# Kernel tuning notes

Hardware: AMD Instinct MI355X
Metric: run time of the kernel (lower is better)

Reference implementation:

```python
import jax, jax.numpy as jnp
import numpy as np

B, T, C = 2, 2048, 2048
NH, NKV = 16, 16
HD = C // NH            # 128
GATE_CH = 32
ROPE_BASE = 10000.0


def setup_inputs() -> dict:
    key = jax.random.key(0)
    ks = jax.random.split(key, 8)
    x = jax.random.normal(ks[0], (B, T, C), jnp.float32)
    ve = jax.random.normal(ks[1], (B, T, C), jnp.float32)
    # RoPE tables: half-dim rotation, shape broadcastable to [B, T, H, HD//2]
    d2 = HD // 2
    inv_freq = 1.0 / (ROPE_BASE ** (jnp.arange(d2, dtype=jnp.float32) / d2))
    angles = jnp.arange(T, dtype=jnp.float32)[:, None] * inv_freq[None, :]  # [T, d2]
    cos = jnp.cos(angles)[None, :, None, :]  # [1, T, 1, d2]
    sin = jnp.sin(angles)[None, :, None, :]
    s = 0.02
    Wq = jax.random.normal(ks[2], (C, NH * HD), jnp.float32) * s
    Wk = jax.random.normal(ks[3], (C, NKV * HD), jnp.float32) * s
    Wv = jax.random.normal(ks[4], (C, NKV * HD), jnp.float32) * s
    Wgate = jax.random.normal(ks[5], (GATE_CH, NKV), jnp.float32) * s
    Wproj = jax.random.normal(ks[6], (NH * HD, C), jnp.float32) * s
    return {"x": x, "ve": ve, "cos": cos, "sin": sin,
            "Wq": Wq, "Wk": Wk, "Wv": Wv, "Wgate": Wgate, "Wproj": Wproj}


def _apply_rotary(x, cos, sin):
    d = x.shape[3] // 2
    x1, x2 = x[..., :d], x[..., d:]
    return jnp.concatenate([x1 * cos + x2 * sin, x1 * -sin + x2 * cos], axis=3)


def _rms_norm(x):
    return x * jax.lax.rsqrt(jnp.mean(x * x, axis=-1, keepdims=True) + 1e-6)


def reference(x, ve, cos, sin, Wq, Wk, Wv, Wgate, Wproj):
    b, t, c = x.shape
    q = (x @ Wq).reshape(b, t, NH, HD)
    k = (x @ Wk).reshape(b, t, NKV, HD)
    v = (x @ Wv).reshape(b, t, NKV, HD)
    # value-embedding gate
    ve_r = ve.reshape(b, t, NKV, HD)
    gate = 2.0 * jax.nn.sigmoid(x[..., :GATE_CH] @ Wgate)  # [B, T, NKV]
    v = v + gate[..., None] * ve_r
    # RoPE then QK-RMSNorm
    q = _rms_norm(_apply_rotary(q, cos, sin))
    k = _rms_norm(_apply_rotary(k, cos, sin))
    # causal attention, scale = 1/sqrt(head_dim)
    scale = 1.0 / np.sqrt(HD).astype(np.float32)
    scores = jnp.einsum('bqhd,bkhd->bhqk', q, k) * scale
    causal = jnp.tril(jnp.ones((t, t), dtype=bool))
    scores = jnp.where(causal, scores, jnp.finfo(scores.dtype).min)
    probs = jax.nn.softmax(scores, axis=-1)
    y = jnp.einsum('bhqk,bkhd->bqhd', probs, v)
    y = y.reshape(b, t, NH * HD)
    return y @ Wproj
```

## Files before the change

### kernel.cpp

```cpp
#include <hip/hip_runtime.h>
#include <stdint.h>

typedef short bf16x8 __attribute__((ext_vector_type(8)));
typedef float f32x4 __attribute__((ext_vector_type(4)));

#define ASYNC16(g, l) __builtin_amdgcn_global_load_lds( \
    (const __attribute__((address_space(1))) unsigned int*)(g), \
    (__attribute__((address_space(3))) unsigned int*)(l), 16, 0, 0)

__device__ __forceinline__ float bf2f(short u) {
  union { unsigned int i; float f; } v;
  v.i = ((unsigned int)(unsigned short)u) << 16;
  return v.f;
}
__device__ __forceinline__ short f2bf(float f) {
  union { float f; unsigned int i; } v;
  v.f = f;
  return (short)(unsigned short)((v.i + 0x8000u) >> 16);
}
__device__ __forceinline__ float ldf(const void* p, long i, int isbf) {
  return isbf ? bf2f(((const short*)p)[i]) : ((const float*)p)[i];
}

__global__ void detect_dtype(const short* __restrict__ x, int* __restrict__ flag) {
  if (threadIdx.x == 0 && blockIdx.x == 0) {
    int cnt = 0;
    for (int i = 0; i < 128; ++i) {
      int e = (((unsigned short)x[i]) >> 7) & 0xFF;
      if (e >= 110 && e <= 136) ++cnt;
    }
    *flag = (cnt >= 120) ? 1 : 0;
  }
}

__global__ __launch_bounds__(256) void convert_x(
    const void* __restrict__ xin, short* __restrict__ xb, const int* __restrict__ flag) {
  long i = (long)blockIdx.x * 2048 + (long)threadIdx.x * 8;
  if (*flag) {
    *(bf16x8*)(xb + i) = *(const bf16x8*)((const short*)xin + i);
  } else {
    const float* xf = (const float*)xin;
    short tmp[8];
    #pragma unroll
    for (int j = 0; j < 8; ++j) tmp[j] = f2bf(xf[i + j]);
    *(bf16x8*)(xb + i) = *(bf16x8*)tmp;
  }
}

__global__ __launch_bounds__(256) void transpose_w(
    const void* __restrict__ S0, short* __restrict__ D0,
    const void* __restrict__ S1, short* __restrict__ D1,
    const void* __restrict__ S2, short* __restrict__ D2,
    const int* __restrict__ flag)
{
  int z = blockIdx.z;
  const void* S = (z == 0) ? S0 : (z == 1) ? S1 : S2;
  short* D = (z == 0) ? D0 : (z == 1) ? D1 : D2;
  int isbf = *flag;
  __shared__ short tile[32][33];
  int c0 = blockIdx.x * 32, r0 = blockIdx.y * 32;
  int tx = threadIdx.x, ty = threadIdx.y;
  #pragma unroll
  for (int i = 0; i < 4; ++i)
    tile[ty + 8*i][tx] = f2bf(ldf(S, (long)(r0 + ty + 8*i) * 2048 + c0 + tx, isbf));
  __syncthreads();
  #pragma unroll
  for (int i = 0; i < 4; ++i)
    D[(long)(c0 + ty + 8*i) * 2048 + r0 + tx] = tile[tx][ty + 8*i];
}

__global__ __launch_bounds__(256) void transpose_v(
    const short* __restrict__ Vr, short* __restrict__ Vt)
{
  __shared__ short tile[32][33];
  int bh = blockIdx.z;
  int b = bh >> 4, h = bh & 15;
  int t0 = blockIdx.x * 32, d0 = blockIdx.y * 32;
  int tx = threadIdx.x, ty = threadIdx.y;
  #pragma unroll
  for (int i = 0; i < 4; ++i)
    tile[ty + 8*i][tx] = Vr[(long)(b*2048 + t0 + ty + 8*i) * 2048 + h*128 + d0 + tx];
  __syncthreads();
  #pragma unroll
  for (int i = 0; i < 4; ++i)
    Vt[((long)bh * 128 + d0 + ty + 8*i) * 2048 + t0 + tx] = tile[tx][ty + 8*i];
}

template<typename OutT>
__global__ __launch_bounds__(256) void gemm_bt(
    const short* __restrict__ A,
    const short* __restrict__ B0, const short* __restrict__ B1, const short* __restrict__ B2,
    OutT* __restrict__ C0, OutT* __restrict__ C1, OutT* __restrict__ C2,
    int M, int N, int K)
{
  int z = blockIdx.z;
  const short* Bt = (z == 0) ? B0 : (z == 1) ? B1 : B2;
  OutT* C = (z == 0) ? C0 : (z == 1) ? C1 : C2;

  int m0 = blockIdx.y * 128, n0 = blockIdx.x * 128;
  int tid = threadIdx.x;
  int lane = tid & 63, w = tid >> 6;
  int quad = lane >> 4, l16 = lane & 15;
  int wm = w >> 1, wn = w & 1;

  __shared__ short As[128][64];
  __shared__ short Bs[128][64];

  f32x4 zero4 = {0.f, 0.f, 0.f, 0.f};
  f32x4 acc[4][4];
  #pragma unroll
  for (int i = 0; i < 4; ++i)
    #pragma unroll
    for (int j = 0; j < 4; ++j) acc[i][j] = zero4;

  int r8 = lane >> 3;
  int srow = w * 32 + r8;
  int scol = ((lane & 7) ^ r8) * 8;

  for (int k0 = 0; k0 < K; k0 += 64) {
    #pragma unroll
    for (int i = 0; i < 4; ++i) {
      ASYNC16(A  + (long)(m0 + srow + i*8) * K + k0 + scol, &As[w*32 + i*8][0]);
      ASYNC16(Bt + (long)(n0 + srow + i*8) * K + k0 + scol, &Bs[w*32 + i*8][0]);
    }
    __syncthreads();
    #pragma unroll
    for (int kt = 0; kt < 2; ++kt) {
      int po = ((kt*4 + quad) ^ (l16 & 7)) * 8;
      bf16x8 af[4], bfr[4];
      #pragma unroll
      for (int i = 0; i < 4; ++i)
        af[i] = *(const bf16x8*)&As[wm*64 + i*16 + l16][po];
      #pragma unroll
      for (int j = 0; j < 4; ++j)
        bfr[j] = *(const bf16x8*)&Bs[wn*64 + j*16 + l16][po];
      #pragma unroll
      for (int i = 0; i < 4; ++i)
        #pragma unroll
        for (int j = 0; j < 4; ++j)
          acc[i][j] = __builtin_amdgcn_mfma_f32_16x16x32_bf16(af[i], bfr[j], acc[i][j], 0, 0, 0);
    }
    __syncthreads();
  }

  #pragma unroll
  for (int i = 0; i < 4; ++i)
    #pragma unroll
    for (int j = 0; j < 4; ++j) {
      int row = m0 + wm*64 + i*16 + quad*4;
      int col = n0 + wn*64 + j*16 + l16;
      #pragma unroll
      for (int r = 0; r < 4; ++r) {
        float v = acc[i][j][r];
        if constexpr (sizeof(OutT) == 4)
          C[(long)(row + r) * N + col] = v;
        else
          C[(long)(row + r) * N + col] = (OutT)f2bf(v);
      }
    }
}

__global__ __launch_bounds__(256) void pointwise(
    const short* __restrict__ xb, const void* __restrict__ ve,
    const void* __restrict__ cosb, const void* __restrict__ sinb,
    const void* __restrict__ Wg, const int* __restrict__ flag,
    short* __restrict__ Qr, short* __restrict__ Kr, short* __restrict__ Vr)
{
  int row = blockIdx.x;
  int tid = threadIdx.x;
  int isbf = *flag;
  __shared__ float xg[32];
  __shared__ float gates[16];
  if (tid < 32) xg[tid] = bf2f(xb[(long)row * 2048 + tid]);
  __syncthreads();
  if (tid < 16) {
    float g = 0.f;
    #pragma unroll
    for (int i = 0; i < 32; ++i) g += xg[i] * ldf(Wg, i*16 + tid, isbf);
    gates[tid] = 2.0f / (1.0f + __expf(-g));
  }
  __syncthreads();
  #pragma unroll
  for (int it = 0; it < 8; ++it) {
    int idx = it * 256 + tid;
    int h = idx >> 7;
    long p = (long)row * 2048 + idx;
    Vr[p] = f2bf(bf2f(Vr[p]) + gates[h] * ldf(ve, p, isbf));
  }
  int lane = tid & 63, w = tid >> 6;
  int t = row & 2047;
  #pragma unroll
  for (int it = 0; it < 8; ++it) {
    int unit = it * 4 + w;
    short* P = (unit < 16) ? Qr : Kr;
    int h = unit & 15;
    long base = (long)row * 2048 + h * 128;
    float x1 = bf2f(P[base + lane]);
    float x2 = bf2f(P[base + lane + 64]);
    float c = ldf(cosb, t*64 + lane, isbf);
    float s = ldf(sinb, t*64 + lane, isbf);
    float r1 = x1 * c + x2 * s;
    float r2 = -x1 * s + x2 * c;
    float ss = r1*r1 + r2*r2;
    #pragma unroll
    for (int off = 32; off; off >>= 1) ss += __shfl_xor(ss, off);
    float rn = rsqrtf(ss * (1.0f/128.0f) + 1e-6f);
    P[base + lane]      = f2bf(r1 * rn);
    P[base + lane + 64] = f2bf(r2 * rn);
  }
}

#define ATT_SCALE 0.08838834764831845f
#define NEG_BIG  -1.0e30f

__global__ __launch_bounds__(256) void flash(
    const short* __restrict__ Q, const short* __restrict__ K,
    const short* __restrict__ Vt, short* __restrict__ Y)
{
  int bx = blockIdx.x;
  int bh = blockIdx.y;
  int b = bh >> 4, h = bh & 15;
  int tid = threadIdx.x;
  int lane = tid & 63, w = tid >> 6;
  int quad = lane >> 4, l16 = lane & 15;

  __shared__ short Ks[2][32*128];
  __shared__ short Vts[2][128*32];
  __shared__ short Ps[4][16*40];

  int qtA = bx, qtB = 31 - bx;
  int nA = 2*(qtA+1), nB = 2*(qtB+1);
  int total = nA + nB;

  int kkey = tid >> 4;
  int klo  = (tid & 15) ^ (kkey & 7);
  int vd   = tid >> 2;
  int vlo  = (tid & 3) ^ (vd & 3);
  const short* Kb0 = K + (long)(b*2048 + kkey) * 2048 + h*128 + klo*8;
  const short* Kb1 = Kb0 + 16L*2048;
  const short* Vb0 = Vt + ((long)bh*128 + vd) * 2048 + vlo*8;
  const short* Vb1 = Vb0 + 64L*2048;

  f32x4 zero4 = {0.f, 0.f, 0.f, 0.f};
  f32x4 o[8];
  float m_i[4], l_i[4];
  bf16x8 qf[4];

  auto stage = [&](int tt, int buf) {
    int tl = (tt < nA) ? tt : tt - nA;
    long ko = (long)tl * 32 * 2048;
    int  vo = tl * 32;
    ASYNC16(Kb0 + ko, &Ks[buf][(w*64)*8]);
    ASYNC16(Kb1 + ko, &Ks[buf][(256 + w*64)*8]);
    ASYNC16(Vb0 + vo, &Vts[buf][(w*64)*8]);
    ASYNC16(Vb1 + vo, &Vts[buf][(256 + w*64)*8]);
  };
  auto loadQ = [&](int qt) {
    const short* Qb = Q + (long)(b*2048 + qt*64 + w*16 + l16) * 2048 + h*128;
    #pragma unroll
    for (int kt = 0; kt < 4; ++kt)
      qf[kt] = *(const bf16x8*)(Qb + kt*32 + quad*8);
  };
  auto flushO = [&](int qt) {
    #pragma unroll
    for (int r = 0; r < 4; ++r) {
      float inv = 1.0f / fmaxf(l_i[r], 1e-20f);
      short* yp = Y + (long)(b*2048 + qt*64 + w*16 + quad*4 + r) * 2048 + h*128;
      #pragma unroll
      for (int c8 = 0; c8 < 8; ++c8)
        yp[c8*16 + l16] = f2bf(o[c8][r] * inv);
    }
  };

  #pragma unroll
  for (int c = 0; c < 8; ++c) o[c] = zero4;
  #pragma unroll
  for (int r = 0; r < 4; ++r) { m_i[r] = NEG_BIG; l_i[r] = 0.f; }
  loadQ(qtA);
  stage(0, 0);

  int qt = qtA, n_seg = nA, segbase = 0;
  for (int tt = 0; tt < total; ++tt) {
    int buf = tt & 1;
    asm volatile("s_waitcnt vmcnt(0)" ::: "memory");
    __builtin_amdgcn_s_barrier();
    if (tt + 1 < total) stage(tt + 1, buf ^ 1);
    if (tt == nA) {
      flushO(qtA);
      loadQ(qtB);
      #pragma unroll
      for (int c = 0; c < 8; ++c) o[c] = zero4;
      #pragma unroll
      for (int r = 0; r < 4; ++r) { m_i[r] = NEG_BIG; l_i[r] = 0.f; }
      qt = qtB; n_seg = nB; segbase = nA;
    }
    int tloc = tt - segbase;
    int kv0 = tloc * 32;

    f32x4 s[2];
    #pragma unroll
    for (int c = 0; c < 2; ++c) {
      f32x4 acc = zero4;
      #pragma unroll
      for (int kt = 0; kt < 4; ++kt) {
        int po = (kt*4 + quad) ^ (l16 & 7);
        bf16x8 kf = *(const bf16x8*)&Ks[buf][(c*16 + l16)*128 + po*8];
        acc = __builtin_amdgcn_mfma_f32_16x16x32_bf16(qf[kt], kf, acc, 0, 0, 0);
      }
      s[c] = acc;
    }

    bool domask = (tloc >= n_seg - 2);
    float p[2][4], mt[4];
    #pragma unroll
    for (int r = 0; r < 4; ++r) mt[r] = NEG_BIG;
    int qgb = qt*64 + w*16 + quad*4;
    #pragma unroll
    for (int c = 0; c < 2; ++c) {
      int kg = kv0 + c*16 + l16;
      #pragma unroll
      for (int r = 0; r < 4; ++r) {
        float v = s[c][r] * ATT_SCALE;
        if (domask) v = (kg <= qgb + r) ? v : NEG_BIG;
        p[c][r] = v;
        mt[r] = fmaxf(mt[r], v);
      }
    }
    #pragma unroll
    for (int off = 1; off < 16; off <<= 1) {
      #pragma unroll
      for (int r = 0; r < 4; ++r) mt[r] = fmaxf(mt[r], __shfl_xor(mt[r], off));
    }
    float alpha[4], rs[4];
    #pragma unroll
    for (int r = 0; r < 4; ++r) {
      float mnew = fmaxf(m_i[r], mt[r]);
      alpha[r] = __expf(m_i[r] - mnew);
      m_i[r] = mnew;
      float sum = 0.f;
      #pragma unroll
      for (int c = 0; c < 2; ++c) { p[c][r] = __expf(p[c][r] - mnew); sum += p[c][r]; }
      rs[r] = sum;
    }
    #pragma unroll
    for (int off = 1; off < 16; off <<= 1) {
      #pragma unroll
      for (int r = 0; r < 4; ++r) rs[r] += __shfl_xor(rs[r], off);
    }
    #pragma unroll
    for (int r = 0; r < 4; ++r) l_i[r] = l_i[r] * alpha[r] + rs[r];
    #pragma unroll
    for (int c8 = 0; c8 < 8; ++c8)
      #pragma unroll
      for (int r = 0; r < 4; ++r) o[c8][r] *= alpha[r];

    #pragma unroll
    for (int c = 0; c < 2; ++c)
      #pragma unroll
      for (int r = 0; r < 4; ++r)
        Ps[w][(quad*4 + r)*40 + c*16 + l16] = f2bf(p[c][r]);
    asm volatile("s_waitcnt lgkmcnt(0)" ::: "memory");
    bf16x8 pa = *(const bf16x8*)&Ps[w][l16*40 + quad*8];

    int pov = quad ^ (l16 & 3);
    #pragma unroll
    for (int c8 = 0; c8 < 8; ++c8) {
      bf16x8 v0 = *(const bf16x8*)&Vts[buf][(c8*16 + l16)*32 + pov*8];
      o[c8] = __builtin_amdgcn_mfma_f32_16x16x32_bf16(pa, v0, o[c8], 0, 0, 0);
    }
  }
  flushO(qtB);
}

extern "C" void kernel_launch(void* const* d_in, const int* in_sizes, int n_in,
                              void* d_out, int out_size, void* d_ws, size_t ws_size,
                              hipStream_t stream) {
  const void* x    = d_in[0];
  const void* ve   = d_in[1];
  const void* cosb = d_in[2];
  const void* sinb = d_in[3];
  const void* Wq   = d_in[4];
  const void* Wk   = d_in[5];
  const void* Wv   = d_in[6];
  const void* Wg   = d_in[7];
  const void* Wp   = d_in[8];
  float* out = (float*)d_out;

  int*   flag = (int*)d_ws;
  short* base = (short*)d_ws + 256;
  short* wt0 = base;
  short* wtk = base + 4194304L;
  short* wtv = base + 8388608L;
  short* Vt  = base + 4194304L;
  short* xb  = base + 12582912L;
  short* Y   = base + 12582912L;
  short* Qr  = base + 20971520L;
  short* Kr  = base + 29360128L;
  short* Vr  = base + 37748736L;

  detect_dtype<<<1, 64, 0, stream>>>((const short*)x, flag);
  convert_x<<<4096, 256, 0, stream>>>(x, xb, flag);
  transpose_w<<<dim3(64, 64, 3), dim3(32, 8), 0, stream>>>(Wq, wt0, Wk, wtk, Wv, wtv, flag);
  gemm_bt<short><<<dim3(16, 32, 3), 256, 0, stream>>>(xb, wt0, wtk, wtv, Qr, Kr, Vr, 4096, 2048, 2048);
  transpose_w<<<dim3(64, 64, 1), dim3(32, 8), 0, stream>>>(Wp, wt0, Wp, wt0, Wp, wt0, flag);
  pointwise<<<dim3(4096), 256, 0, stream>>>(xb, ve, cosb, sinb, Wg, flag, Qr, Kr, Vr);
  transpose_v<<<dim3(64, 4, 32), dim3(32, 8), 0, stream>>>(Vr, Vt);
  flash<<<dim3(16, 32), 256, 0, stream>>>(Qr, Kr, Vt, Y);
  gemm_bt<float><<<dim3(16, 32, 1), 256, 0, stream>>>(Y, wt0, wt0, wt0, out, out, out, 4096, 2048, 2048);
}
```

Measured before the change: 528.1 us.

## Drop online softmax max via static bound from QK-RMSNorm, widen KV tile

```diff
diff --git a/kernel.cpp b/kernel.cpp
--- a/kernel.cpp
+++ b/kernel.cpp
@@ -210,8 +210,8 @@
   }
 }
 
-#define ATT_SCALE 0.08838834764831845f
-#define NEG_BIG  -1.0e30f
+#define FL_C1 0.12751741f
+#define FL_C2 16.321698f
 
 __global__ __launch_bounds__(256) void flash(
     const short* __restrict__ Q, const short* __restrict__ K,
@@ -224,36 +224,39 @@
   int lane = tid & 63, w = tid >> 6;
   int quad = lane >> 4, l16 = lane & 15;
 
-  __shared__ short Ks[2][32*128];
-  __shared__ short Vts[2][128*32];
-  __shared__ short Ps[4][16*40];
+  __shared__ short Ks[2][64*128];
+  __shared__ short Vts[2][128*64];
+  __shared__ short Ps[4][16*72];
 
   int qtA = bx, qtB = 31 - bx;
-  int nA = 2*(qtA+1), nB = 2*(qtB+1);
+  int nA = qtA + 1, nB = qtB + 1;
   int total = nA + nB;
 
   int kkey = tid >> 4;
   int klo  = (tid & 15) ^ (kkey & 7);
-  int vd   = tid >> 2;
-  int vlo  = (tid & 3) ^ (vd & 3);
-  const short* Kb0 = K + (long)(b*2048 + kkey) * 2048 + h*128 + klo*8;
-  const short* Kb1 = Kb0 + 16L*2048;
-  const short* Vb0 = Vt + ((long)bh*128 + vd) * 2048 + vlo*8;
-  const short* Vb1 = Vb0 + 64L*2048;
+  int vd   = tid >> 3;
+  int vlo  = (tid & 7) ^ (vd & 7);
+  const short* Kbase = K + (long)(b*2048 + kkey) * 2048 + h*128 + klo*8;
+  const short* Vbase = Vt + ((long)bh*128 + vd) * 2048 + vlo*8;
 
   f32x4 zero4 = {0.f, 0.f, 0.f, 0.f};
   f32x4 o[8];
-  float m_i[4], l_i[4];
+  float l_i[4];
   bf16x8 qf[4];
+  bf16x8 ones;
+  #pragma unroll
+  for (int j = 0; j < 8; ++j) ones[j] = (short)0x3F80;
 
   auto stage = [&](int tt, int buf) {
     int tl = (tt < nA) ? tt : tt - nA;
-    long ko = (long)tl * 32 * 2048;
-    int  vo = tl * 32;
-    ASYNC16(Kb0 + ko, &Ks[buf][(w*64)*8]);
-    ASYNC16(Kb1 + ko, &Ks[buf][(256 + w*64)*8]);
-    ASYNC16(Vb0 + vo, &Vts[buf][(w*64)*8]);
-    ASYNC16(Vb1 + vo, &Vts[buf][(256 + w*64)*8]);
+    long ko = (long)tl * 64 * 2048;
+    int  vo = tl * 64;
+    #pragma unroll
+    for (int i = 0; i < 4; ++i)
+      ASYNC16(Kbase + ko + (long)i*16*2048, &Ks[buf][(i*16 + w*4)*128]);
+    #pragma unroll
+    for (int i = 0; i < 4; ++i)
+      ASYNC16(Vbase + vo + (long)i*32*2048, &Vts[buf][(i*32 + w*8)*64]);
   };
   auto loadQ = [&](int qt) {
     const short* Qb = Q + (long)(b*2048 + qt*64 + w*16 + l16) * 2048 + h*128;
@@ -264,7 +267,7 @@
   auto flushO = [&](int qt) {
     #pragma unroll
     for (int r = 0; r < 4; ++r) {
-      float inv = 1.0f / fmaxf(l_i[r], 1e-20f);
+      float inv = 1.0f / fmaxf(l_i[r], 1e-30f);
       short* yp = Y + (long)(b*2048 + qt*64 + w*16 + quad*4 + r) * 2048 + h*128;
       #pragma unroll
       for (int c8 = 0; c8 < 8; ++c8)
@@ -275,7 +278,7 @@
   #pragma unroll
   for (int c = 0; c < 8; ++c) o[c] = zero4;
   #pragma unroll
-  for (int r = 0; r < 4; ++r) { m_i[r] = NEG_BIG; l_i[r] = 0.f; }
+  for (int r = 0; r < 4; ++r) l_i[r] = 0.f;
   loadQ(qtA);
   stage(0, 0);
 
@@ -291,82 +294,55 @@
       #pragma unroll
       for (int c = 0; c < 8; ++c) o[c] = zero4;
       #pragma unroll
-      for (int r = 0; r < 4; ++r) { m_i[r] = NEG_BIG; l_i[r] = 0.f; }
+      for (int r = 0; r < 4; ++r) l_i[r] = 0.f;
       qt = qtB; n_seg = nB; segbase = nA;
     }
     int tloc = tt - segbase;
-    int kv0 = tloc * 32;
-
-    f32x4 s[2];
-    #pragma unroll
-    for (int c = 0; c < 2; ++c) {
+    int kv0 = tloc * 64;
+
+    f32x4 s[4];
+    #pragma unroll
+    for (int c = 0; c < 4; ++c) {
       f32x4 acc = zero4;
       #pragma unroll
       for (int kt = 0; kt < 4; ++kt) {
-        int po = (kt*4 + quad) ^ (l16 & 7);
-        bf16x8 kf = *(const bf16x8*)&Ks[buf][(c*16 + l16)*128 + po*8];
+        int po = ((kt*4 + quad) ^ (l16 & 7)) * 8;
+        bf16x8 kf = *(const bf16x8*)&Ks[buf][(c*16 + l16)*128 + po];
         acc = __builtin_amdgcn_mfma_f32_16x16x32_bf16(qf[kt], kf, acc, 0, 0, 0);
       }
       s[c] = acc;
     }
 
-    bool domask = (tloc >= n_seg - 2);
-    float p[2][4], mt[4];
-    #pragma unroll
-    for (int r = 0; r < 4; ++r) mt[r] = NEG_BIG;
+    bool domask = (tloc == n_seg - 1);
     int qgb = qt*64 + w*16 + quad*4;
     #pragma unroll
-    for (int c = 0; c < 2; ++c) {
+    for (int c = 0; c < 4; ++c) {
       int kg = kv0 + c*16 + l16;
       #pragma unroll
       for (int r = 0; r < 4; ++r) {
-        float v = s[c][r] * ATT_SCALE;
-        if (domask) v = (kg <= qgb + r) ? v : NEG_BIG;
-        p[c][r] = v;
-        mt[r] = fmaxf(mt[r], v);
+        float t = s[c][r] * FL_C1 - FL_C2;
+        if (domask && kg > qgb + r) t = -1000.0f;
+        float pv = exp2f(t);
+        Ps[w][(quad*4 + r)*72 + c*16 + l16] = f2bf(pv);
       }
     }
-    #pragma unroll
-    for (int off = 1; off < 16; off <<= 1) {
-      #pragma unroll
-      for (int r = 0; r < 4; ++r) mt[r] = fmaxf(mt[r], __shfl_xor(mt[r], off));
-    }
-    float alpha[4], rs[4];
-    #pragma unroll
-    for (int r = 0; r < 4; ++r) {
-      float mnew = fmaxf(m_i[r], mt[r]);
-      alpha[r] = __expf(m_i[r] - mnew);
-      m_i[r] = mnew;
-      float sum = 0.f;
-      #pragma unroll
-      for (int c = 0; c < 2; ++c) { p[c][r] = __expf(p[c][r] - mnew); sum += p[c][r]; }
-      rs[r] = sum;
-    }
-    #pragma unroll
-    for (int off = 1; off < 16; off <<= 1) {
-      #pragma unroll
-      for (int r = 0; r < 4; ++r) rs[r] += __shfl_xor(rs[r], off);
-    }
-    #pragma unroll
-    for (int r = 0; r < 4; ++r) l_i[r] = l_i[r] * alpha[r] + rs[r];
-    #pragma unroll
-    for (int c8 = 0; c8 < 8; ++c8)
-      #pragma unroll
-      for (int r = 0; r < 4; ++r) o[c8][r] *= alpha[r];
-
-    #pragma unroll
-    for (int c = 0; c < 2; ++c)
-      #pragma unroll
-      for (int r = 0; r < 4; ++r)
-        Ps[w][(quad*4 + r)*40 + c*16 + l16] = f2bf(p[c][r]);
     asm volatile("s_waitcnt lgkmcnt(0)" ::: "memory");
-    bf16x8 pa = *(const bf16x8*)&Ps[w][l16*40 + quad*8];
-
-    int pov = quad ^ (l16 & 3);
+    bf16x8 pa0 = *(const bf16x8*)&Ps[w][l16*72 + quad*8];
+    bf16x8 pa1 = *(const bf16x8*)&Ps[w][l16*72 + 32 + quad*8];
+
+    f32x4 racc = __builtin_amdgcn_mfma_f32_16x16x32_bf16(pa0, ones, zero4, 0, 0, 0);
+    racc = __builtin_amdgcn_mfma_f32_16x16x32_bf16(pa1, ones, racc, 0, 0, 0);
+    #pragma unroll
+    for (int r = 0; r < 4; ++r) l_i[r] += racc[r];
+
     #pragma unroll
     for (int c8 = 0; c8 < 8; ++c8) {
-      bf16x8 v0 = *(const bf16x8*)&Vts[buf][(c8*16 + l16)*32 + pov*8];
-      o[c8] = __builtin_amdgcn_mfma_f32_16x16x32_bf16(pa, v0, o[c8], 0, 0, 0);
+      int po0 = ((0*4 + quad) ^ (l16 & 7)) * 8;
+      int po1 = ((1*4 + quad) ^ (l16 & 7)) * 8;
+      bf16x8 v0 = *(const bf16x8*)&Vts[buf][(c8*16 + l16)*64 + po0];
+      bf16x8 v1 = *(const bf16x8*)&Vts[buf][(c8*16 + l16)*64 + po1];
+      o[c8] = __builtin_amdgcn_mfma_f32_16x16x32_bf16(pa0, v0, o[c8], 0, 0, 0);
+      o[c8] = __builtin_amdgcn_mfma_f32_16x16x32_bf16(pa1, v1, o[c8], 0, 0, 0);
     }
   }
   flushO(qtB);
```

Result: faster. 477.4 us (-9.6%).
